# Performance work log

Measured on AMD Instinct MI355X. Metric: run time of the kernel, lower is better.

The kernel has to match this reference:

```python
import jax, jax.numpy as jnp
import numpy as np

# RadixAttention EXTEND forward: queries over newly-extended tokens attend to
# (a) the full cached prefix KV (non-causal) and (b) the extend-token KV (causal),
# equivalent to attention over concat([prefix, extend]) with a shifted causal mask.

SCALING = 0.08838834764831845  # 1/sqrt(128)


def setup_inputs() -> dict:
    key = jax.random.key(0)
    k1, k2, k3, k4, k5 = jax.random.split(key, 5)
    B, E, P, H, Hk, D = 4, 512, 1536, 32, 8, 128
    return {
        "q": jax.random.normal(k1, (B, E, H, D), dtype=jnp.float32),
        "k": jax.random.normal(k2, (B, E, Hk, D), dtype=jnp.float32),
        "v": jax.random.normal(k3, (B, E, Hk, D), dtype=jnp.float32),
        "k_cache": jax.random.normal(k4, (B, P, Hk, D), dtype=jnp.float32),
        "v_cache": jax.random.normal(k5, (B, P, Hk, D), dtype=jnp.float32),
    }


def reference(q, k, v, k_cache, v_cache):
    B, E, H, D = q.shape
    Hk = k.shape[2]
    P = k_cache.shape[1]
    g = H // Hk  # GQA group size
    S = P + E

    k_all = jnp.concatenate([k_cache, k], axis=1)  # [B, S, Hk, D]
    v_all = jnp.concatenate([v_cache, v], axis=1)  # [B, S, Hk, D]

    qg = q.reshape(B, E, Hk, g, D)
    # scores: [B, Hk, g, E, S]
    scores = jnp.einsum("bekgd,bskd->bkges", qg, k_all) * SCALING

    # key j visible to extend-query e iff j <= P + e (prefix fully visible, extend causal)
    visible = jnp.arange(S)[None, :] <= (P + jnp.arange(E))[:, None]  # [E, S]
    scores = jnp.where(visible[None, None, None, :, :], scores, jnp.float32(-1e30))

    p = jax.nn.softmax(scores, axis=-1)
    o = jnp.einsum("bkges,bskd->bekgd", p, v_all).reshape(B, E, H, D)
    # module returns flat [num_tokens, H*D]
    return o.reshape(B * E, H * D)
```

## Files before the change

### kernel.cpp

```cpp
#include <hip/hip_runtime.h>
#include <hip/hip_bf16.h>
#include <stdint.h>
#include <stddef.h>


#define B_ 4
#define E_ 512
#define P_ 1536
#define H_ 32
#define HK_ 8
#define D_ 128
#define G_ 4
#define S_ 2048

#define BLOCK_E 64
#define NT 64
#define KPITCH 136
#define VPITCH 72
#define PPITCH 72
#define KVSTRIDE (HK_ * D_)
#define NTHREADS 1024

typedef __attribute__((ext_vector_type(8))) short short8v;
typedef __attribute__((ext_vector_type(4))) float floatx4;

__device__ __forceinline__ short2 f2bf2(float a, float b) {
  __hip_bfloat162 h = __float22bfloat162_rn(float2{a, b});
  return *(short2*)&h;
}
__device__ __forceinline__ short f2bf(float f) {
  union { float f; uint32_t u; } x; x.f = f;
  uint32_t r = x.u + 0x7FFFu + ((x.u >> 16) & 1u);
  return (short)(r >> 16);
}
__device__ __forceinline__ short8v cvt8(const float4 a, const float4 b) {
  short2 p0 = f2bf2(a.x, a.y), p1 = f2bf2(a.z, a.w);
  short2 p2 = f2bf2(b.x, b.y), p3 = f2bf2(b.z, b.w);
  short8v f;
  f[0] = p0.x; f[1] = p0.y; f[2] = p1.x; f[3] = p1.y;
  f[4] = p2.x; f[5] = p2.y; f[6] = p3.x; f[7] = p3.y;
  return f;
}

__global__ __launch_bounds__(256)
void prep_k(const float* __restrict__ kc, const float* __restrict__ ke,
            short* __restrict__ kb) {
  const int cid = blockIdx.x * 256 + threadIdx.x;
  const int d8c = cid & 15;
  const int j   = (cid >> 4) & (S_ - 1);
  const int kh  = (cid >> 15) & 7;
  const int b   = cid >> 18;
  const float* src = (j < P_)
      ? (kc + (((size_t)b * P_ + j) * HK_ + kh) * D_ + d8c * 8)
      : (ke + (((size_t)b * E_ + (j - P_)) * HK_ + kh) * D_ + d8c * 8);
  const float4 x0 = *(const float4*)src;
  const float4 x1 = *(const float4*)(src + 4);
  *(short8v*)&kb[(((size_t)b * HK_ + kh) * S_ + j) * D_ + d8c * 8] = cvt8(x0, x1);
}

__global__ __launch_bounds__(256)
void prep_v(const float* __restrict__ vc, const float* __restrict__ ve,
            short* __restrict__ vt) {
  __shared__ short TT[D_ * VPITCH];
  const int j0 = blockIdx.x * 64;
  const int kh = blockIdx.y;
  const int b  = blockIdx.z;
  const int tid = threadIdx.x;
#pragma unroll
  for (int it = 0; it < 8; ++it) {
    const int linear = it * 256 + tid;
    const int key = linear >> 5;
    const int dof = (linear & 31) * 4;
    const int j = j0 + key;
    const float* src = (j < P_)
        ? (vc + (((size_t)b * P_ + j) * HK_ + kh) * D_ + dof)
        : (ve + (((size_t)b * E_ + (j - P_)) * HK_ + kh) * D_ + dof);
    const float4 x = *(const float4*)src;
    short2 a = f2bf2(x.x, x.y), c = f2bf2(x.z, x.w);
    TT[(dof + 0) * VPITCH + key] = a.x;
    TT[(dof + 1) * VPITCH + key] = a.y;
    TT[(dof + 2) * VPITCH + key] = c.x;
    TT[(dof + 3) * VPITCH + key] = c.y;
  }
  __syncthreads();
#pragma unroll
  for (int it = 0; it < 4; ++it) {
    const int linear = it * 256 + tid;
    const int d  = linear >> 3;
    const int k8 = (linear & 7) * 8;
    const short8v y = *(const short8v*)&TT[d * VPITCH + k8];
    *(short8v*)&vt[(((size_t)b * HK_ + kh) * D_ + d) * S_ + j0 + k8] = y;
  }
}

template <bool PRE>
__global__ __launch_bounds__(NTHREADS, 4)
void radix_extend_attn(const float* __restrict__ q,
                       const float* __restrict__ ke,
                       const float* __restrict__ ve,
                       const float* __restrict__ kc,
                       const float* __restrict__ vc,
                       const short* __restrict__ kb,
                       const short* __restrict__ vt,
                       float* __restrict__ out) {
  __shared__ short KT[NT * KPITCH];
  __shared__ short VT[D_ * VPITCH];
  __shared__ short PW[16][16 * PPITCH];

  const int flat = blockIdx.x;
  const int kh   = flat & 7;
  const int b    = (flat >> 3) & 3;
  const int e0   = (flat >> 5) * BLOCK_E;
  const int tid  = threadIdx.x;
  const int wave = tid >> 6;
  const int lane = tid & 63;
  const int quad = lane >> 4;
  const int l16  = lane & 15;
  const int gi   = wave & 3;
  const int rbw  = wave >> 2;
  const int h    = kh * G_ + gi;

  short8v qf[4];
  {
    const int e = e0 + rbw * 16 + l16;
    const float* qp = q + (((size_t)b * E_ + e) * H_ + h) * D_ + quad * 8;
#pragma unroll
    for (int kcc = 0; kcc < 4; ++kcc)
      qf[kcc] = cvt8(*(const float4*)(qp + kcc * 32), *(const float4*)(qp + kcc * 32 + 4));
  }

  short8v ones8;
#pragma unroll
  for (int i = 0; i < 8; ++i) ones8[i] = (l16 == 0) ? (short)0x3F80 : (short)0;

  floatx4 oacc[8];
#pragma unroll
  for (int dvc = 0; dvc < 8; ++dvc) oacc[dvc] = (floatx4){0.f, 0.f, 0.f, 0.f};
  floatx4 acc_l = (floatx4){0.f, 0.f, 0.f, 0.f};
  float mrow[4];
#pragma unroll
  for (int r = 0; r < 4; ++r) mrow[r] = -1e30f;

  const int slimit = P_ + e0 + BLOCK_E;
  const int ntiles = slimit / NT;
  const float sc = 0.08838834764831845f * 1.44269504088896340f;

  const int kkey = tid >> 4;
  const int kd8  = (tid & 15) * 8;
  const int vd   = tid >> 3;
  const int vk8  = (tid & 7) * 8;

  const short* kbb = kb + ((size_t)b * HK_ + kh) * S_ * D_;
  const short* vtb = vt + ((size_t)b * HK_ + kh) * (size_t)D_ * S_;
  const float* kcb = kc + (size_t)b * P_ * KVSTRIDE + (size_t)kh * D_;
  const float* keb = ke + (size_t)b * E_ * KVSTRIDE + (size_t)kh * D_;
  const float* vcb = vc + (size_t)b * P_ * KVSTRIDE + (size_t)kh * D_;
  const float* veb = ve + (size_t)b * E_ * KVSTRIDE + (size_t)kh * D_;

  short8v kpre8, vpre8;
  float4 kpre[2], vpre[2];

  auto preload = [&](int kt0n) {
    if (PRE) {
      kpre8 = *(const short8v*)&kbb[(size_t)(kt0n + kkey) * D_ + kd8];
      vpre8 = *(const short8v*)&vtb[(size_t)vd * S_ + kt0n + vk8];
    } else {
#pragma unroll
      for (int it = 0; it < 2; ++it) {
        const int linear = it * NTHREADS + tid;
        const int key = linear >> 5, dof = (linear & 31) * 4;
        const int j = kt0n + key;
        const float* src = (j < P_) ? (kcb + (size_t)j * KVSTRIDE)
                                    : (keb + (size_t)(j - P_) * KVSTRIDE);
        kpre[it] = *(const float4*)(src + dof);
      }
#pragma unroll
      for (int it = 0; it < 2; ++it) {
        const int linear = it * NTHREADS + tid;
        const int key = linear & 63, dg = (linear >> 6) * 4;
        const int j = kt0n + key;
        const float* src = (j < P_) ? (vcb + (size_t)j * KVSTRIDE)
                                    : (veb + (size_t)(j - P_) * KVSTRIDE);
        vpre[it] = *(const float4*)(src + dg);
      }
    }
  };

  preload(0);

  for (int t = 0; t < ntiles; ++t) {
    const int kt0 = t * NT;

    if (PRE) {
      *(short8v*)&KT[kkey * KPITCH + kd8] = kpre8;
      *(short8v*)&VT[vd * VPITCH + vk8]   = vpre8;
    } else {
#pragma unroll
      for (int it = 0; it < 2; ++it) {
        const int linear = it * NTHREADS + tid;
        const int key = linear >> 5, dof = (linear & 31) * 4;
        short2 a = f2bf2(kpre[it].x, kpre[it].y), c = f2bf2(kpre[it].z, kpre[it].w);
        short4 y; y.x = a.x; y.y = a.y; y.z = c.x; y.w = c.y;
        *(short4*)&KT[key * KPITCH + dof] = y;
      }
#pragma unroll
      for (int it = 0; it < 2; ++it) {
        const int linear = it * NTHREADS + tid;
        const int key = linear & 63, dg = (linear >> 6) * 4;
        short2 a = f2bf2(vpre[it].x, vpre[it].y), c = f2bf2(vpre[it].z, vpre[it].w);
        VT[(dg + 0) * VPITCH + key] = a.x;
        VT[(dg + 1) * VPITCH + key] = a.y;
        VT[(dg + 2) * VPITCH + key] = c.x;
        VT[(dg + 3) * VPITCH + key] = c.y;
      }
    }
    __syncthreads();

    if (t + 1 < ntiles) preload(kt0 + NT);

    floatx4 sfr[4];
#pragma unroll
    for (int nc = 0; nc < 4; ++nc) {
      floatx4 acc = (floatx4){0.f, 0.f, 0.f, 0.f};
#pragma unroll
      for (int kcc = 0; kcc < 4; ++kcc) {
        const short8v bf = *(const short8v*)&KT[(nc * 16 + l16) * KPITCH + kcc * 32 + quad * 8];
        acc = __builtin_amdgcn_mfma_f32_16x16x32_bf16(qf[kcc], bf, acc, 0, 0, 0);
      }
      sfr[nc] = acc;
    }

    const bool need_mask = (kt0 + NT - 1 > P_ + e0 + rbw * 16);
#pragma unroll
    for (int nc = 0; nc < 4; ++nc)
#pragma unroll
      for (int reg = 0; reg < 4; ++reg) {
        float s = sfr[nc][reg] * sc;
        if (need_mask) {
          const int jkey = kt0 + nc * 16 + l16;
          const int erow = e0 + rbw * 16 + quad * 4 + reg;
          if (jkey > P_ + erow) s = -1e30f;
        }
        sfr[nc][reg] = s;
      }

    float mt[4];
#pragma unroll
    for (int reg = 0; reg < 4; ++reg)
      mt[reg] = fmaxf(fmaxf(sfr[0][reg], sfr[1][reg]), fmaxf(sfr[2][reg], sfr[3][reg]));
#pragma unroll
    for (int off = 1; off < 16; off <<= 1)
#pragma unroll
      for (int reg = 0; reg < 4; ++reg)
        mt[reg] = fmaxf(mt[reg], __shfl_xor(mt[reg], off, 64));

#pragma unroll
    for (int reg = 0; reg < 4; ++reg) {
      const float mnew = fmaxf(mrow[reg], mt[reg]);
      const float alpha = __builtin_amdgcn_exp2f(mrow[reg] - mnew);
      mrow[reg] = mnew;
      acc_l[reg] *= alpha;
#pragma unroll
      for (int dvc = 0; dvc < 8; ++dvc) oacc[dvc][reg] *= alpha;
    }

#pragma unroll
    for (int nc = 0; nc < 4; ++nc)
#pragma unroll
      for (int reg = 0; reg < 4; ++reg) {
        const float p = __builtin_amdgcn_exp2f(sfr[nc][reg] - mrow[reg]);
        PW[wave][(quad * 4 + reg) * PPITCH + nc * 16 + l16] = f2bf(p);
      }

    const short8v pf0 = *(const short8v*)&PW[wave][l16 * PPITCH + quad * 8];
    const short8v pf1 = *(const short8v*)&PW[wave][l16 * PPITCH + 32 + quad * 8];
#pragma unroll
    for (int dvc = 0; dvc < 8; ++dvc) {
      const short8v vf0 = *(const short8v*)&VT[(dvc * 16 + l16) * VPITCH + quad * 8];
      const short8v vf1 = *(const short8v*)&VT[(dvc * 16 + l16) * VPITCH + 32 + quad * 8];
      oacc[dvc] = __builtin_amdgcn_mfma_f32_16x16x32_bf16(pf0, vf0, oacc[dvc], 0, 0, 0);
      oacc[dvc] = __builtin_amdgcn_mfma_f32_16x16x32_bf16(pf1, vf1, oacc[dvc], 0, 0, 0);
    }
    acc_l = __builtin_amdgcn_mfma_f32_16x16x32_bf16(pf0, ones8, acc_l, 0, 0, 0);
    acc_l = __builtin_amdgcn_mfma_f32_16x16x32_bf16(pf1, ones8, acc_l, 0, 0, 0);
    __syncthreads();
  }

  float inv[4];
#pragma unroll
  for (int reg = 0; reg < 4; ++reg) {
    const float l = __shfl(acc_l[reg], lane & 48, 64);
    inv[reg] = 1.0f / l;
  }
#pragma unroll
  for (int reg = 0; reg < 4; ++reg) {
    const int erow = e0 + rbw * 16 + quad * 4 + reg;
    float* op = out + (size_t)(b * E_ + erow) * (H_ * D_) + h * D_ + l16;
#pragma unroll
    for (int dvc = 0; dvc < 8; ++dvc)
      op[dvc * 16] = oacc[dvc][reg] * inv[reg];
  }
}

extern "C" void kernel_launch(void* const* d_in, const int* in_sizes, int n_in,
                              void* d_out, int out_size, void* d_ws, size_t ws_size,
                              hipStream_t stream) {
  const float* q  = (const float*)d_in[0];
  const float* ke = (const float*)d_in[1];
  const float* ve = (const float*)d_in[2];
  const float* kc = (const float*)d_in[3];
  const float* vc = (const float*)d_in[4];
  float* out = (float*)d_out;

  const size_t kv_shorts = (size_t)B_ * HK_ * S_ * D_;
  const size_t need = 2 * kv_shorts * sizeof(short);
  const int nblk = (E_ / BLOCK_E) * HK_ * B_;

  if (ws_size >= need) {
    short* kb = (short*)d_ws;
    short* vt = kb + kv_shorts;
    prep_k<<<dim3((unsigned)(kv_shorts / 8 / 256)), dim3(256), 0, stream>>>(kc, ke, kb);
    prep_v<<<dim3(S_ / 64, HK_, B_), dim3(256), 0, stream>>>(vc, ve, vt);
    radix_extend_attn<true><<<dim3(nblk), dim3(NTHREADS), 0, stream>>>(
        q, ke, ve, kc, vc, kb, vt, out);
  } else {
    radix_extend_attn<false><<<dim3(nblk), dim3(NTHREADS), 0, stream>>>(
        q, ke, ve, kc, vc, nullptr, nullptr, out);
  }
}
```

Baseline: 256.1 us.

## Restructure attention kernel into 256-thread blocks with double-buffered swizzled LDS

The main attention kernel now uses 256-thread blocks with one wave per GQA head. Each wave handles two 16-row query blocks (BLOCK_E 32), so every K/V fragment read from LDS feeds two MFMA chains. K is staged through an XOR-swizzled, unpadded LDS layout and V through a double-buffered swizzled layout, with the next tile prefetched two steps ahead to overlap global loads with compute. This doubles the grid to more, smaller blocks and raises register pressure. The fp32 fallback path is split into its own kernel with no prefetch.

New measurement: 246.6 us. 1.04x faster.

```diff
diff --git a/kernel.cpp b/kernel.cpp
--- a/kernel.cpp
+++ b/kernel.cpp
@@ -13,13 +13,12 @@
 #define G_ 4
 #define S_ 2048
 
-#define BLOCK_E 64
+#define BLOCK_E 32
 #define NT 64
-#define KPITCH 136
-#define VPITCH 72
-#define PPITCH 72
+#define PPITCH 80
+#define TPITCH 72
 #define KVSTRIDE (HK_ * D_)
-#define NTHREADS 1024
+#define NTHREADS 256
 
 typedef __attribute__((ext_vector_type(8))) short short8v;
 typedef __attribute__((ext_vector_type(4))) float floatx4;
@@ -61,7 +60,7 @@
 __global__ __launch_bounds__(256)
 void prep_v(const float* __restrict__ vc, const float* __restrict__ ve,
             short* __restrict__ vt) {
-  __shared__ short TT[D_ * VPITCH];
+  __shared__ short TT[D_ * TPITCH];
   const int j0 = blockIdx.x * 64;
   const int kh = blockIdx.y;
   const int b  = blockIdx.z;
@@ -77,10 +76,10 @@
         : (ve + (((size_t)b * E_ + (j - P_)) * HK_ + kh) * D_ + dof);
     const float4 x = *(const float4*)src;
     short2 a = f2bf2(x.x, x.y), c = f2bf2(x.z, x.w);
-    TT[(dof + 0) * VPITCH + key] = a.x;
-    TT[(dof + 1) * VPITCH + key] = a.y;
-    TT[(dof + 2) * VPITCH + key] = c.x;
-    TT[(dof + 3) * VPITCH + key] = c.y;
+    TT[(dof + 0) * TPITCH + key] = a.x;
+    TT[(dof + 1) * TPITCH + key] = a.y;
+    TT[(dof + 2) * TPITCH + key] = c.x;
+    TT[(dof + 3) * TPITCH + key] = c.y;
   }
   __syncthreads();
 #pragma unroll
@@ -88,24 +87,19 @@
     const int linear = it * 256 + tid;
     const int d  = linear >> 3;
     const int k8 = (linear & 7) * 8;
-    const short8v y = *(const short8v*)&TT[d * VPITCH + k8];
+    const short8v y = *(const short8v*)&TT[d * TPITCH + k8];
     *(short8v*)&vt[(((size_t)b * HK_ + kh) * D_ + d) * S_ + j0 + k8] = y;
   }
 }
 
-template <bool PRE>
-__global__ __launch_bounds__(NTHREADS, 4)
-void radix_extend_attn(const float* __restrict__ q,
-                       const float* __restrict__ ke,
-                       const float* __restrict__ ve,
-                       const float* __restrict__ kc,
-                       const float* __restrict__ vc,
-                       const short* __restrict__ kb,
-                       const short* __restrict__ vt,
-                       float* __restrict__ out) {
-  __shared__ short KT[NT * KPITCH];
-  __shared__ short VT[D_ * VPITCH];
-  __shared__ short PW[16][16 * PPITCH];
+__global__ __launch_bounds__(NTHREADS, 2)
+void radix_attn(const float* __restrict__ q,
+                const short* __restrict__ kb,
+                const short* __restrict__ vt,
+                float* __restrict__ out) {
+  __shared__ short KT[NT * D_];
+  __shared__ short VT[2][D_ * NT];
+  __shared__ short PW[4][32 * PPITCH];
 
   const int flat = blockIdx.x;
   const int kh   = flat & 7;
@@ -116,10 +110,213 @@
   const int lane = tid & 63;
   const int quad = lane >> 4;
   const int l16  = lane & 15;
-  const int gi   = wave & 3;
-  const int rbw  = wave >> 2;
-  const int h    = kh * G_ + gi;
-
+  const int h    = kh * G_ + wave;
+
+  short8v qf[2][4];
+#pragma unroll
+  for (int rb = 0; rb < 2; ++rb) {
+    const int e = e0 + rb * 16 + l16;
+    const float* qp = q + (((size_t)b * E_ + e) * H_ + h) * D_ + quad * 8;
+#pragma unroll
+    for (int kcc = 0; kcc < 4; ++kcc)
+      qf[rb][kcc] = cvt8(*(const float4*)(qp + kcc * 32), *(const float4*)(qp + kcc * 32 + 4));
+  }
+
+  short8v ones8;
+#pragma unroll
+  for (int i = 0; i < 8; ++i) ones8[i] = (l16 == 0) ? (short)0x3F80 : (short)0;
+
+  floatx4 oacc[2][8];
+#pragma unroll
+  for (int rb = 0; rb < 2; ++rb)
+#pragma unroll
+    for (int dvc = 0; dvc < 8; ++dvc) oacc[rb][dvc] = (floatx4){0.f, 0.f, 0.f, 0.f};
+  floatx4 acc_l[2] = {(floatx4){0.f, 0.f, 0.f, 0.f}, (floatx4){0.f, 0.f, 0.f, 0.f}};
+  float mrow[2][4];
+#pragma unroll
+  for (int rb = 0; rb < 2; ++rb)
+#pragma unroll
+    for (int r = 0; r < 4; ++r) mrow[rb][r] = -1e30f;
+
+  const short* kbb = kb + ((size_t)b * HK_ + kh) * S_ * D_;
+  const short* vtb = vt + ((size_t)b * HK_ + kh) * (size_t)D_ * S_;
+
+  const int slimit = P_ + e0 + BLOCK_E;
+  const int ntiles = (slimit + NT - 1) / NT;
+  const float sc = 0.08838834764831845f * 1.44269504088896340f;
+
+  short8v kpre[4], vpre[4];
+  auto preload = [&](int t) {
+    const int kt0 = t * NT;
+#pragma unroll
+    for (int it = 0; it < 4; ++it) {
+      const int c = it * 256 + tid;
+      const int key = c >> 4, cl = c & 15;
+      kpre[it] = *(const short8v*)&kbb[(size_t)(kt0 + key) * D_ + cl * 8];
+    }
+#pragma unroll
+    for (int it = 0; it < 4; ++it) {
+      const int c = it * 256 + tid;
+      const int d = c >> 3, ck = c & 7;
+      vpre[it] = *(const short8v*)&vtb[(size_t)d * S_ + kt0 + ck * 8];
+    }
+  };
+  auto stage = [&](int buf) {
+#pragma unroll
+    for (int it = 0; it < 4; ++it) {
+      const int c = it * 256 + tid;
+      const int key = c >> 4, cl = c & 15;
+      const int cs = ((cl & 7) ^ (key & 7)) | (cl & 8);
+      *(short8v*)&KT[key * D_ + cs * 8] = kpre[it];
+    }
+#pragma unroll
+    for (int it = 0; it < 4; ++it) {
+      const int c = it * 256 + tid;
+      const int d = c >> 3, ck = c & 7;
+      *(short8v*)&VT[buf][d * NT + (ck ^ (d & 7)) * 8] = vpre[it];
+    }
+  };
+
+  preload(0);
+  stage(0);
+  if (ntiles > 1) preload(1);
+  __syncthreads();
+
+  for (int t = 0; t < ntiles; ++t) {
+    const int kt0 = t * NT;
+    const int cur = t & 1;
+
+    floatx4 sfr[2][4];
+#pragma unroll
+    for (int nc = 0; nc < 4; ++nc) {
+      short8v bfr[4];
+#pragma unroll
+      for (int kcc = 0; kcc < 4; ++kcc) {
+        const int cl = 4 * kcc + quad;
+        const int cs = ((cl & 7) ^ (l16 & 7)) | (cl & 8);
+        bfr[kcc] = *(const short8v*)&KT[(nc * 16 + l16) * D_ + cs * 8];
+      }
+#pragma unroll
+      for (int rb = 0; rb < 2; ++rb) {
+        floatx4 acc = (floatx4){0.f, 0.f, 0.f, 0.f};
+#pragma unroll
+        for (int kcc = 0; kcc < 4; ++kcc)
+          acc = __builtin_amdgcn_mfma_f32_16x16x32_bf16(qf[rb][kcc], bfr[kcc], acc, 0, 0, 0);
+        sfr[rb][nc] = acc;
+      }
+    }
+    __syncthreads();
+
+    if (t + 1 < ntiles) stage((t + 1) & 1);
+    if (t + 2 < ntiles) preload(t + 2);
+
+#pragma unroll
+    for (int rb = 0; rb < 2; ++rb) {
+      const bool need_mask = (kt0 + NT - 1 > P_ + e0 + rb * 16);
+#pragma unroll
+      for (int nc = 0; nc < 4; ++nc)
+#pragma unroll
+        for (int reg = 0; reg < 4; ++reg) {
+          float s = sfr[rb][nc][reg] * sc;
+          if (need_mask) {
+            const int jkey = kt0 + nc * 16 + l16;
+            const int erow = e0 + rb * 16 + quad * 4 + reg;
+            if (jkey > P_ + erow) s = -1e30f;
+          }
+          sfr[rb][nc][reg] = s;
+        }
+      float mt[4];
+#pragma unroll
+      for (int reg = 0; reg < 4; ++reg)
+        mt[reg] = fmaxf(fmaxf(sfr[rb][0][reg], sfr[rb][1][reg]),
+                        fmaxf(sfr[rb][2][reg], sfr[rb][3][reg]));
+#pragma unroll
+      for (int off = 1; off < 16; off <<= 1)
+#pragma unroll
+        for (int reg = 0; reg < 4; ++reg)
+          mt[reg] = fmaxf(mt[reg], __shfl_xor(mt[reg], off, 64));
+#pragma unroll
+      for (int reg = 0; reg < 4; ++reg) {
+        const float mnew = fmaxf(mrow[rb][reg], mt[reg]);
+        const float alpha = __builtin_amdgcn_exp2f(mrow[rb][reg] - mnew);
+        mrow[rb][reg] = mnew;
+        acc_l[rb][reg] *= alpha;
+#pragma unroll
+        for (int dvc = 0; dvc < 8; ++dvc) oacc[rb][dvc][reg] *= alpha;
+      }
+#pragma unroll
+      for (int reg = 0; reg < 4; ++reg) {
+        const float p0 = __builtin_amdgcn_exp2f(sfr[rb][0][reg] - mrow[rb][reg]);
+        const float p1 = __builtin_amdgcn_exp2f(sfr[rb][1][reg] - mrow[rb][reg]);
+        const float p2 = __builtin_amdgcn_exp2f(sfr[rb][2][reg] - mrow[rb][reg]);
+        const float p3 = __builtin_amdgcn_exp2f(sfr[rb][3][reg] - mrow[rb][reg]);
+        const short2 a = f2bf2(p0, p1), c = f2bf2(p2, p3);
+        short* pw = &PW[wave][(rb * 16 + quad * 4 + reg) * PPITCH + l16];
+        pw[0] = a.x; pw[16] = a.y; pw[32] = c.x; pw[48] = c.y;
+      }
+    }
+
+    short8v pf[2][2];
+#pragma unroll
+    for (int rb = 0; rb < 2; ++rb)
+#pragma unroll
+      for (int c2 = 0; c2 < 2; ++c2)
+        pf[rb][c2] = *(const short8v*)&PW[wave][(rb * 16 + l16) * PPITCH + c2 * 32 + quad * 8];
+#pragma unroll
+    for (int dvc = 0; dvc < 8; ++dvc) {
+      const int rd = dvc * 16 + l16;
+      const int cs0 = (quad ^ (l16 & 7));
+      const int cs1 = ((4 + quad) ^ (l16 & 7));
+      const short8v vf0 = *(const short8v*)&VT[cur][rd * NT + cs0 * 8];
+      const short8v vf1 = *(const short8v*)&VT[cur][rd * NT + cs1 * 8];
+#pragma unroll
+      for (int rb = 0; rb < 2; ++rb) {
+        oacc[rb][dvc] = __builtin_amdgcn_mfma_f32_16x16x32_bf16(pf[rb][0], vf0, oacc[rb][dvc], 0, 0, 0);
+        oacc[rb][dvc] = __builtin_amdgcn_mfma_f32_16x16x32_bf16(pf[rb][1], vf1, oacc[rb][dvc], 0, 0, 0);
+      }
+    }
+#pragma unroll
+    for (int rb = 0; rb < 2; ++rb) {
+      acc_l[rb] = __builtin_amdgcn_mfma_f32_16x16x32_bf16(pf[rb][0], ones8, acc_l[rb], 0, 0, 0);
+      acc_l[rb] = __builtin_amdgcn_mfma_f32_16x16x32_bf16(pf[rb][1], ones8, acc_l[rb], 0, 0, 0);
+    }
+    __syncthreads();
+  }
+
+#pragma unroll
+  for (int rb = 0; rb < 2; ++rb) {
+    float inv[4];
+#pragma unroll
+    for (int reg = 0; reg < 4; ++reg) {
+      const float l = __shfl(acc_l[rb][reg], lane & 48, 64);
+      inv[reg] = 1.0f / l;
+    }
+#pragma unroll
+    for (int reg = 0; reg < 4; ++reg) {
+      const int erow = e0 + rb * 16 + quad * 4 + reg;
+      float* op = out + (size_t)(b * E_ + erow) * (H_ * D_) + h * D_ + l16;
+#pragma unroll
+      for (int dvc = 0; dvc < 8; ++dvc)
+        op[dvc * 16] = oacc[rb][dvc][reg] * inv[reg];
+    }
+  }
+}
+
+__global__ __launch_bounds__(1024, 4)
+void radix_attn_fp32(const float* __restrict__ q,
+                     const float* __restrict__ ke,
+                     const float* __restrict__ ve,
+                     const float* __restrict__ kc,
+                     const float* __restrict__ vc,
+                     float* __restrict__ out) {
+  __shared__ short KT[NT * 136];
+  __shared__ short VTs[D_ * TPITCH];
+  __shared__ short PW[16][16 * PPITCH];
+  const int flat = blockIdx.x;
+  const int kh = flat & 7, b = (flat >> 3) & 3, e0 = (flat >> 5) * 64;
+  const int tid = threadIdx.x, wave = tid >> 6, lane = tid & 63;
+  const int quad = lane >> 4, l16 = lane & 15;
+  const int gi = wave & 3, rbw = wave >> 2, h = kh * G_ + gi;
   short8v qf[4];
   {
     const int e = e0 + rbw * 16 + l16;
@@ -128,108 +325,61 @@
     for (int kcc = 0; kcc < 4; ++kcc)
       qf[kcc] = cvt8(*(const float4*)(qp + kcc * 32), *(const float4*)(qp + kcc * 32 + 4));
   }
-
   short8v ones8;
 #pragma unroll
   for (int i = 0; i < 8; ++i) ones8[i] = (l16 == 0) ? (short)0x3F80 : (short)0;
-
   floatx4 oacc[8];
 #pragma unroll
-  for (int dvc = 0; dvc < 8; ++dvc) oacc[dvc] = (floatx4){0.f, 0.f, 0.f, 0.f};
+  for (int d = 0; d < 8; ++d) oacc[d] = (floatx4){0.f, 0.f, 0.f, 0.f};
   floatx4 acc_l = (floatx4){0.f, 0.f, 0.f, 0.f};
   float mrow[4];
 #pragma unroll
   for (int r = 0; r < 4; ++r) mrow[r] = -1e30f;
-
-  const int slimit = P_ + e0 + BLOCK_E;
-  const int ntiles = slimit / NT;
-  const float sc = 0.08838834764831845f * 1.44269504088896340f;
-
-  const int kkey = tid >> 4;
-  const int kd8  = (tid & 15) * 8;
-  const int vd   = tid >> 3;
-  const int vk8  = (tid & 7) * 8;
-
-  const short* kbb = kb + ((size_t)b * HK_ + kh) * S_ * D_;
-  const short* vtb = vt + ((size_t)b * HK_ + kh) * (size_t)D_ * S_;
   const float* kcb = kc + (size_t)b * P_ * KVSTRIDE + (size_t)kh * D_;
   const float* keb = ke + (size_t)b * E_ * KVSTRIDE + (size_t)kh * D_;
   const float* vcb = vc + (size_t)b * P_ * KVSTRIDE + (size_t)kh * D_;
   const float* veb = ve + (size_t)b * E_ * KVSTRIDE + (size_t)kh * D_;
-
-  short8v kpre8, vpre8;
-  float4 kpre[2], vpre[2];
-
-  auto preload = [&](int kt0n) {
-    if (PRE) {
-      kpre8 = *(const short8v*)&kbb[(size_t)(kt0n + kkey) * D_ + kd8];
-      vpre8 = *(const short8v*)&vtb[(size_t)vd * S_ + kt0n + vk8];
-    } else {
-#pragma unroll
-      for (int it = 0; it < 2; ++it) {
-        const int linear = it * NTHREADS + tid;
-        const int key = linear >> 5, dof = (linear & 31) * 4;
-        const int j = kt0n + key;
-        const float* src = (j < P_) ? (kcb + (size_t)j * KVSTRIDE)
-                                    : (keb + (size_t)(j - P_) * KVSTRIDE);
-        kpre[it] = *(const float4*)(src + dof);
-      }
-#pragma unroll
-      for (int it = 0; it < 2; ++it) {
-        const int linear = it * NTHREADS + tid;
-        const int key = linear & 63, dg = (linear >> 6) * 4;
-        const int j = kt0n + key;
-        const float* src = (j < P_) ? (vcb + (size_t)j * KVSTRIDE)
-                                    : (veb + (size_t)(j - P_) * KVSTRIDE);
-        vpre[it] = *(const float4*)(src + dg);
-      }
-    }
-  };
-
-  preload(0);
-
+  const int ntiles = (P_ + e0 + 64) / NT;
+  const float sc = 0.08838834764831845f * 1.44269504088896340f;
   for (int t = 0; t < ntiles; ++t) {
     const int kt0 = t * NT;
-
-    if (PRE) {
-      *(short8v*)&KT[kkey * KPITCH + kd8] = kpre8;
-      *(short8v*)&VT[vd * VPITCH + vk8]   = vpre8;
-    } else {
-#pragma unroll
-      for (int it = 0; it < 2; ++it) {
-        const int linear = it * NTHREADS + tid;
-        const int key = linear >> 5, dof = (linear & 31) * 4;
-        short2 a = f2bf2(kpre[it].x, kpre[it].y), c = f2bf2(kpre[it].z, kpre[it].w);
-        short4 y; y.x = a.x; y.y = a.y; y.z = c.x; y.w = c.y;
-        *(short4*)&KT[key * KPITCH + dof] = y;
-      }
-#pragma unroll
-      for (int it = 0; it < 2; ++it) {
-        const int linear = it * NTHREADS + tid;
-        const int key = linear & 63, dg = (linear >> 6) * 4;
-        short2 a = f2bf2(vpre[it].x, vpre[it].y), c = f2bf2(vpre[it].z, vpre[it].w);
-        VT[(dg + 0) * VPITCH + key] = a.x;
-        VT[(dg + 1) * VPITCH + key] = a.y;
-        VT[(dg + 2) * VPITCH + key] = c.x;
-        VT[(dg + 3) * VPITCH + key] = c.y;
-      }
-    }
     __syncthreads();
-
-    if (t + 1 < ntiles) preload(kt0 + NT);
-
+#pragma unroll
+    for (int it = 0; it < 2; ++it) {
+      const int linear = it * 1024 + tid;
+      const int key = linear >> 5, dof = (linear & 31) * 4;
+      const int j = kt0 + key;
+      const float* src = (j < P_) ? (kcb + (size_t)j * KVSTRIDE) : (keb + (size_t)(j - P_) * KVSTRIDE);
+      const float4 x = *(const float4*)(src + dof);
+      short2 a = f2bf2(x.x, x.y), c = f2bf2(x.z, x.w);
+      short4 y; y.x = a.x; y.y = a.y; y.z = c.x; y.w = c.y;
+      *(short4*)&KT[key * 136 + dof] = y;
+    }
+#pragma unroll
+    for (int it = 0; it < 2; ++it) {
+      const int linear = it * 1024 + tid;
+      const int key = linear & 63, dg = (linear >> 6) * 4;
+      const int j = kt0 + key;
+      const float* src = (j < P_) ? (vcb + (size_t)j * KVSTRIDE) : (veb + (size_t)(j - P_) * KVSTRIDE);
+      const float4 x = *(const float4*)(src + dg);
+      short2 a = f2bf2(x.x, x.y), c = f2bf2(x.z, x.w);
+      VTs[(dg + 0) * TPITCH + key] = a.x;
+      VTs[(dg + 1) * TPITCH + key] = a.y;
+      VTs[(dg + 2) * TPITCH + key] = c.x;
+      VTs[(dg + 3) * TPITCH + key] = c.y;
+    }
+    __syncthreads();
     floatx4 sfr[4];
 #pragma unroll
     for (int nc = 0; nc < 4; ++nc) {
       floatx4 acc = (floatx4){0.f, 0.f, 0.f, 0.f};
 #pragma unroll
       for (int kcc = 0; kcc < 4; ++kcc) {
-        const short8v bf = *(const short8v*)&KT[(nc * 16 + l16) * KPITCH + kcc * 32 + quad * 8];
+        const short8v bf = *(const short8v*)&KT[(nc * 16 + l16) * 136 + kcc * 32 + quad * 8];
         acc = __builtin_amdgcn_mfma_f32_16x16x32_bf16(qf[kcc], bf, acc, 0, 0, 0);
       }
       sfr[nc] = acc;
     }
-
     const bool need_mask = (kt0 + NT - 1 > P_ + e0 + rbw * 16);
 #pragma unroll
     for (int nc = 0; nc < 4; ++nc)
@@ -243,7 +393,6 @@
         }
         sfr[nc][reg] = s;
       }
-
     float mt[4];
 #pragma unroll
     for (int reg = 0; reg < 4; ++reg)
@@ -253,7 +402,6 @@
 #pragma unroll
       for (int reg = 0; reg < 4; ++reg)
         mt[reg] = fmaxf(mt[reg], __shfl_xor(mt[reg], off, 64));
-
 #pragma unroll
     for (int reg = 0; reg < 4; ++reg) {
       const float mnew = fmaxf(mrow[reg], mt[reg]);
@@ -261,9 +409,8 @@
       mrow[reg] = mnew;
       acc_l[reg] *= alpha;
 #pragma unroll
-      for (int dvc = 0; dvc < 8; ++dvc) oacc[dvc][reg] *= alpha;
-    }
-
+      for (int d = 0; d < 8; ++d) oacc[d][reg] *= alpha;
+    }
 #pragma unroll
     for (int nc = 0; nc < 4; ++nc)
 #pragma unroll
@@ -271,34 +418,29 @@
         const float p = __builtin_amdgcn_exp2f(sfr[nc][reg] - mrow[reg]);
         PW[wave][(quad * 4 + reg) * PPITCH + nc * 16 + l16] = f2bf(p);
       }
-
     const short8v pf0 = *(const short8v*)&PW[wave][l16 * PPITCH + quad * 8];
     const short8v pf1 = *(const short8v*)&PW[wave][l16 * PPITCH + 32 + quad * 8];
 #pragma unroll
-    for (int dvc = 0; dvc < 8; ++dvc) {
-      const short8v vf0 = *(const short8v*)&VT[(dvc * 16 + l16) * VPITCH + quad * 8];
-      const short8v vf1 = *(const short8v*)&VT[(dvc * 16 + l16) * VPITCH + 32 + quad * 8];
-      oacc[dvc] = __builtin_amdgcn_mfma_f32_16x16x32_bf16(pf0, vf0, oacc[dvc], 0, 0, 0);
-      oacc[dvc] = __builtin_amdgcn_mfma_f32_16x16x32_bf16(pf1, vf1, oacc[dvc], 0, 0, 0);
+    for (int d = 0; d < 8; ++d) {
+      const short8v vf0 = *(const short8v*)&VTs[(d * 16 + l16) * TPITCH + quad * 8];
+      const short8v vf1 = *(const short8v*)&VTs[(d * 16 + l16) * TPITCH + 32 + quad * 8];
+      oacc[d] = __builtin_amdgcn_mfma_f32_16x16x32_bf16(pf0, vf0, oacc[d], 0, 0, 0);
+      oacc[d] = __builtin_amdgcn_mfma_f32_16x16x32_bf16(pf1, vf1, oacc[d], 0, 0, 0);
     }
     acc_l = __builtin_amdgcn_mfma_f32_16x16x32_bf16(pf0, ones8, acc_l, 0, 0, 0);
     acc_l = __builtin_amdgcn_mfma_f32_16x16x32_bf16(pf1, ones8, acc_l, 0, 0, 0);
-    __syncthreads();
-  }
-
+  }
   float inv[4];
 #pragma unroll
-  for (int reg = 0; reg < 4; ++reg) {
-    const float l = __shfl(acc_l[reg], lane & 48, 64);
-    inv[reg] = 1.0f / l;
-  }
+  for (int reg = 0; reg < 4; ++reg)
+    inv[reg] = 1.0f / __shfl(acc_l[reg], lane & 48, 64);
 #pragma unroll
   for (int reg = 0; reg < 4; ++reg) {
     const int erow = e0 + rbw * 16 + quad * 4 + reg;
     float* op = out + (size_t)(b * E_ + erow) * (H_ * D_) + h * D_ + l16;
 #pragma unroll
-    for (int dvc = 0; dvc < 8; ++dvc)
-      op[dvc * 16] = oacc[dvc][reg] * inv[reg];
+    for (int d = 0; d < 8; ++d)
+      op[d * 16] = oacc[d][reg] * inv[reg];
   }
 }
 
@@ -314,17 +456,15 @@
 
   const size_t kv_shorts = (size_t)B_ * HK_ * S_ * D_;
   const size_t need = 2 * kv_shorts * sizeof(short);
-  const int nblk = (E_ / BLOCK_E) * HK_ * B_;
 
   if (ws_size >= need) {
     short* kb = (short*)d_ws;
     short* vt = kb + kv_shorts;
     prep_k<<<dim3((unsigned)(kv_shorts / 8 / 256)), dim3(256), 0, stream>>>(kc, ke, kb);
     prep_v<<<dim3(S_ / 64, HK_, B_), dim3(256), 0, stream>>>(vc, ve, vt);
-    radix_extend_attn<true><<<dim3(nblk), dim3(NTHREADS), 0, stream>>>(
-        q, ke, ve, kc, vc, kb, vt, out);
+    const int nblk = (E_ / BLOCK_E) * HK_ * B_;
+    radix_attn<<<dim3(nblk), dim3(NTHREADS), 0, stream>>>(q, kb, vt, out);
   } else {
-    radix_extend_attn<false><<<dim3(nblk), dim3(NTHREADS), 0, stream>>>(
-        q, ke, ve, kc, vc, nullptr, nullptr, out);
-  }
-}
+    radix_attn_fp32<<<dim3(8 * 8 * 4), dim3(1024), 0, stream>>>(q, ke, ve, kc, vc, out);
+  }
+}
```
